# Kernel optimization log

Measured on AMD Instinct MI355X. Metric: run time of the kernel, lower is better.

## Reference

```python
import jax, jax.numpy as jnp
import numpy as np

B, S, D, E, K = 4, 2048, 2048, 64, 2

def setup_inputs() -> dict:
    key = jax.random.key(0)
    k1, k2, k3, k4 = jax.random.split(key, 4)
    x = jax.random.normal(k1, (B, S, D), dtype=jnp.float32)
    W = jax.random.normal(k2, (E, D), dtype=jnp.float32) * 0.02  # gate_linear.weight
    noise_weight = jax.random.normal(k3, (E,), dtype=jnp.float32) * 0.02
    noise = jax.random.normal(k4, (B, S, E), dtype=jnp.float32)  # torch.randn_like(logits), noisy_std=1.0
    return {"x": x, "W": W, "noise_weight": noise_weight, "noise": noise, "k": K}

def reference(x, W, noise_weight, noise, k):
    # logits = x @ W.T  -> [B, S, E]
    logits = jnp.einsum('bsd,ed->bse', x, W)
    # noise injection: randn * noisy_std(=1.0) * noise_weight (per-expert scale)
    logits_noisy = logits + noise * noise_weight
    # top-k over experts
    top_vals, top_idx = jax.lax.top_k(logits_noisy, k)  # [B, S, k]
    # softmax over a tensor that is -inf everywhere except the top-k slots is
    # exactly: zeros everywhere, softmax(top_vals) scattered into the top-k slots.
    probs = jax.nn.softmax(top_vals, axis=-1)  # [B, S, k]
    n_tok = B * S
    rows = jnp.arange(n_tok)[:, None]  # [n_tok, 1]
    gated = jnp.zeros((n_tok, E), dtype=logits.dtype)
    gated = gated.at[rows, top_idx.reshape(n_tok, k)].set(probs.reshape(n_tok, k))
    gated = gated.reshape(B, S, E)
    return gated, top_idx, top_vals
```

## Files before the change

kernel.cpp:

```cpp
#include <hip/hip_runtime.h>
#include <math.h>

#define NTOK 8192
#define DDIM 2048
#define NEXP 64
#define MT   16
#define ASTR 72
#define CSTR 68

#define GATED_SZ (NTOK * NEXP)
#define IDX_OFF  GATED_SZ
#define VALS_OFF (GATED_SZ + NTOK * 2)

#define NKSTEP (DDIM / 32)
#define NTILE  (NEXP / 16)
#define BFRAG_HALVES ((size_t)NKSTEP * NTILE * 64 * 8)

typedef _Float16 f16x8 __attribute__((ext_vector_type(8)));
typedef _Float16 f16x4 __attribute__((ext_vector_type(4)));
typedef float    f32x4 __attribute__((ext_vector_type(4)));

__global__ void pack_b_kernel(const float* __restrict__ W,
                              _Float16* __restrict__ Bh,
                              _Float16* __restrict__ Bl)
{
    const int tid  = blockIdx.x * blockDim.x + threadIdx.x;
    const int lane = tid & 63;
    const int fid  = tid >> 6;
    const int ks   = fid >> 2;
    const int nt   = fid & 3;
    const int e    = nt * 16 + (lane & 15);
    const int k    = ks * 32 + (lane >> 4) * 8;
    const float* src = W + (size_t)e * DDIM + k;

    f16x8 hi, lo;
#pragma unroll
    for (int j = 0; j < 8; ++j) {
        const float v = src[j];
        const _Float16 h = (_Float16)v;
        hi[j] = h;
        lo[j] = (_Float16)((v - (float)h) * 4096.f);
    }
    *(f16x8*)(Bh + (size_t)tid * 8) = hi;
    *(f16x8*)(Bl + (size_t)tid * 8) = lo;
}

#define BFRAG(base, ks, nt) \
    (*(const f16x8*)((base) + ((((size_t)(ks)) * 4 + (nt)) * 64 + lane) * 8))

static __device__ __forceinline__ void cvt_hilo4(float4 v, f16x4& h4, f16x4& l4)
{
    const float vv[4] = {v.x, v.y, v.z, v.w};
#pragma unroll
    for (int j = 0; j < 4; ++j) {
        const _Float16 hh = (_Float16)vv[j];
        h4[j] = hh;
        l4[j] = (_Float16)((vv[j] - (float)hh) * 4096.f);
    }
}

__global__ __launch_bounds__(512, 4) void gate_kernel(
    const float* __restrict__ x,
    const _Float16* __restrict__ Bh,
    const _Float16* __restrict__ Bl,
    const float* __restrict__ noise_w,
    const float* __restrict__ noise,
    float* __restrict__ out)
{
    __shared__ __align__(16) char smem_raw[8 * 2 * MT * ASTR * 2];

    const int tid  = threadIdx.x;
    const int lane = tid & 63;
    const int w    = __builtin_amdgcn_readfirstlane(tid >> 6);
    const int tokBase = blockIdx.x * MT;

    const int q = lane >> 4;
    const int m = lane & 15;

    _Float16* xs = (_Float16*)smem_raw + (size_t)w * (2 * MT * ASTR);

    const float* xw = x + (size_t)tokBase * DDIM + (size_t)w * 256;

    const float nwv = noise_w[lane];
    const float nz0 = noise[(size_t)(tokBase + w * 2)     * NEXP + lane];
    const float nz1 = noise[(size_t)(tokBase + w * 2 + 1) * NEXP + lane];

    f32x4 acc_hh[4], acc_lo[4];
#pragma unroll
    for (int nt = 0; nt < 4; ++nt) {
        acc_hh[nt] = (f32x4){0.f, 0.f, 0.f, 0.f};
        acc_lo[nt] = (f32x4){0.f, 0.f, 0.f, 0.f};
    }

#define LOADSUB(buf, s)                                                      \
    _Pragma("unroll")                                                        \
    for (int p = 0; p < 4; ++p) {                                            \
        buf[p] = *(const float4*)(xw + (size_t)(p * 4 + q) * DDIM            \
                                  + (s) * 64 + m * 4);                       \
    }

#define STAGESUB(buf)                                                        \
    _Pragma("unroll")                                                        \
    for (int p = 0; p < 4; ++p) {                                            \
        f16x4 h4, l4;                                                        \
        cvt_hilo4(buf[p], h4, l4);                                           \
        const int off = (p * 4 + q) * ASTR + m * 4;                          \
        *(f16x4*)&xs[off] = h4;                                              \
        *(f16x4*)&xs[MT * ASTR + off] = l4;                                  \
    }

#define COMPUTESUB(s)                                                        \
    _Pragma("unroll")                                                        \
    for (int stp = 0; stp < 2; ++stp) {                                      \
        const int ks = w * 8 + (s) * 2 + stp;                                \
        const f16x8 ah = *(const f16x8*)&xs[m * ASTR + stp * 32 + q * 8];    \
        const f16x8 al = *(const f16x8*)&xs[MT * ASTR + m * ASTR + stp * 32 + q * 8]; \
        _Pragma("unroll")                                                    \
        for (int nt = 0; nt < 4; ++nt) {                                     \
            const f16x8 bh = BFRAG(Bh, ks, nt);                              \
            const f16x8 bl = BFRAG(Bl, ks, nt);                              \
            acc_hh[nt] = __builtin_amdgcn_mfma_f32_16x16x32_f16(ah, bh, acc_hh[nt], 0, 0, 0); \
            acc_lo[nt] = __builtin_amdgcn_mfma_f32_16x16x32_f16(ah, bl, acc_lo[nt], 0, 0, 0); \
            acc_lo[nt] = __builtin_amdgcn_mfma_f32_16x16x32_f16(al, bh, acc_lo[nt], 0, 0, 0); \
        }                                                                    \
    }

    float4 rA[4], rB[4];
    LOADSUB(rA, 0)
    LOADSUB(rB, 1)
    STAGESUB(rA)
    LOADSUB(rA, 2)
    COMPUTESUB(0)
    STAGESUB(rB)
    LOADSUB(rB, 3)
    COMPUTESUB(1)
    STAGESUB(rA)
    COMPUTESUB(2)
    STAGESUB(rB)
    COMPUTESUB(3)

#undef LOADSUB
#undef STAGESUB
#undef COMPUTESUB

    __syncthreads();
    float* cbuf = (float*)smem_raw;

#pragma unroll
    for (int nt = 0; nt < 4; ++nt) {
        const int e = nt * 16 + m;
#pragma unroll
        for (int r = 0; r < 4; ++r) {
            const int t = q * 4 + r;
            cbuf[((w * MT) + t) * CSTR + e] = acc_hh[nt][r] + acc_lo[nt][r] * (1.f / 4096.f);
        }
    }
    __syncthreads();

#pragma unroll
    for (int i = 0; i < 2; ++i) {
        const int t   = w * 2 + i;
        const int tok = tokBase + t;
        const int e   = lane;

        float v = 0.f;
#pragma unroll
        for (int p = 0; p < 8; ++p)
            v += cbuf[((p * MT) + t) * CSTR + e];
        v += (i ? nz1 : nz0) * nwv;

        float m1 = v; int i1 = e;
#pragma unroll
        for (int sh = 32; sh > 0; sh >>= 1) {
            float ov = __shfl_xor(m1, sh, 64);
            int   oi = __shfl_xor(i1, sh, 64);
            if (ov > m1 || (ov == m1 && oi < i1)) { m1 = ov; i1 = oi; }
        }
        float vm = (e == i1) ? -INFINITY : v;
        float m2 = vm; int i2 = e;
#pragma unroll
        for (int sh = 32; sh > 0; sh >>= 1) {
            float ov = __shfl_xor(m2, sh, 64);
            int   oi = __shfl_xor(i2, sh, 64);
            if (ov > m2 || (ov == m2 && oi < i2)) { m2 = ov; i2 = oi; }
        }

        const float e2  = expf(m2 - m1);
        const float inv = 1.f / (1.f + e2);
        const float p1  = inv;
        const float p2  = e2 * inv;

        float gval = 0.f;
        if (e == i1) gval = p1;
        else if (e == i2) gval = p2;
        out[(size_t)tok * NEXP + e] = gval;

        if (lane == 0) {
            out[IDX_OFF  + tok * 2 + 0] = (float)i1;
            out[IDX_OFF  + tok * 2 + 1] = (float)i2;
            out[VALS_OFF + tok * 2 + 0] = m1;
            out[VALS_OFF + tok * 2 + 1] = m2;
        }
    }
}

extern "C" void kernel_launch(void* const* d_in, const int* in_sizes, int n_in,
                              void* d_out, int out_size, void* d_ws, size_t ws_size,
                              hipStream_t stream) {
    const float* x     = (const float*)d_in[0];
    const float* W     = (const float*)d_in[1];
    const float* nw    = (const float*)d_in[2];
    const float* noise = (const float*)d_in[3];
    float* out = (float*)d_out;

    _Float16* Bh = (_Float16*)d_ws;
    _Float16* Bl = Bh + BFRAG_HALVES;

    hipLaunchKernelGGL(pack_b_kernel, dim3(64), dim3(256), 0, stream, W, Bh, Bl);

    hipLaunchKernelGGL(gate_kernel, dim3(NTOK / MT), dim3(512), 0, stream,
                       x, Bh, Bl, nw, noise, out);
}
```

Baseline: 112.8 us.

## Double token tile to 32 and split K across 16 waves per block

Each block now handles 32 tokens with 1024 threads (16 waves), and each wave covers a 128-wide K slice with two 16-row M tiles. The point is to reuse each loaded W fragment across twice as many tokens, which halves the global/L2 traffic for B per token. In exchange the K-split reduction now sums 16 partials, shared memory grows, and load/compute pipelining drops from double to single buffering. Launching 1024-thread blocks with launch_bounds(1024,4) may also limit registers and occupancy.

```diff
diff --git a/kernel.cpp b/kernel.cpp
--- a/kernel.cpp
+++ b/kernel.cpp
@@ -4,9 +4,11 @@
 #define NTOK 8192
 #define DDIM 2048
 #define NEXP 64
-#define MT   16
-#define ASTR 72
-#define CSTR 68
+#define MT   32
+#define ASTR 40
+#define XLO  (32 * ASTR)
+#define WST  (2 * 32 * ASTR)
+#define CSTR 66
 
 #define GATED_SZ (NTOK * NEXP)
 #define IDX_OFF  GATED_SZ
@@ -59,7 +61,7 @@
     }
 }
 
-__global__ __launch_bounds__(512, 4) void gate_kernel(
+__global__ __launch_bounds__(1024, 4) void gate_kernel(
     const float* __restrict__ x,
     const _Float16* __restrict__ Bh,
     const _Float16* __restrict__ Bl,
@@ -67,7 +69,7 @@
     const float* __restrict__ noise,
     float* __restrict__ out)
 {
-    __shared__ __align__(16) char smem_raw[8 * 2 * MT * ASTR * 2];
+    __shared__ __align__(16) char smem_raw[16 * 32 * CSTR * 4];
 
     const int tid  = threadIdx.x;
     const int lane = tid & 63;
@@ -77,66 +79,72 @@
     const int q = lane >> 4;
     const int m = lane & 15;
 
-    _Float16* xs = (_Float16*)smem_raw + (size_t)w * (2 * MT * ASTR);
-
-    const float* xw = x + (size_t)tokBase * DDIM + (size_t)w * 256;
+    _Float16* xs = (_Float16*)smem_raw + (size_t)w * WST;
+
+    const int srow = tid & 0 ? 0 : (lane >> 3);
+    const int scol = (lane & 7) * 4;
+    const float* xw = x + (size_t)tokBase * DDIM + (size_t)w * 128;
 
     const float nwv = noise_w[lane];
     const float nz0 = noise[(size_t)(tokBase + w * 2)     * NEXP + lane];
     const float nz1 = noise[(size_t)(tokBase + w * 2 + 1) * NEXP + lane];
 
-    f32x4 acc_hh[4], acc_lo[4];
-#pragma unroll
-    for (int nt = 0; nt < 4; ++nt) {
-        acc_hh[nt] = (f32x4){0.f, 0.f, 0.f, 0.f};
-        acc_lo[nt] = (f32x4){0.f, 0.f, 0.f, 0.f};
-    }
-
-#define LOADSUB(buf, s)                                                      \
+    f32x4 acc_hh[2][4], acc_lo[2][4];
+#pragma unroll
+    for (int mt = 0; mt < 2; ++mt)
+#pragma unroll
+        for (int nt = 0; nt < 4; ++nt) {
+            acc_hh[mt][nt] = (f32x4){0.f, 0.f, 0.f, 0.f};
+            acc_lo[mt][nt] = (f32x4){0.f, 0.f, 0.f, 0.f};
+        }
+
+#define LOADSUB(s)                                                           \
     _Pragma("unroll")                                                        \
     for (int p = 0; p < 4; ++p) {                                            \
-        buf[p] = *(const float4*)(xw + (size_t)(p * 4 + q) * DDIM            \
-                                  + (s) * 64 + m * 4);                       \
-    }
-
-#define STAGESUB(buf)                                                        \
+        rA[p] = *(const float4*)(xw + (size_t)(p * 8 + srow) * DDIM          \
+                                 + (s) * 32 + scol);                         \
+    }
+
+#define STAGESUB()                                                           \
     _Pragma("unroll")                                                        \
     for (int p = 0; p < 4; ++p) {                                            \
         f16x4 h4, l4;                                                        \
-        cvt_hilo4(buf[p], h4, l4);                                           \
-        const int off = (p * 4 + q) * ASTR + m * 4;                          \
+        cvt_hilo4(rA[p], h4, l4);                                            \
+        const int off = (p * 8 + srow) * ASTR + scol;                        \
         *(f16x4*)&xs[off] = h4;                                              \
-        *(f16x4*)&xs[MT * ASTR + off] = l4;                                  \
+        *(f16x4*)&xs[XLO + off] = l4;                                        \
     }
 
 #define COMPUTESUB(s)                                                        \
-    _Pragma("unroll")                                                        \
-    for (int stp = 0; stp < 2; ++stp) {                                      \
-        const int ks = w * 8 + (s) * 2 + stp;                                \
-        const f16x8 ah = *(const f16x8*)&xs[m * ASTR + stp * 32 + q * 8];    \
-        const f16x8 al = *(const f16x8*)&xs[MT * ASTR + m * ASTR + stp * 32 + q * 8]; \
+    {                                                                        \
+        const int ks = w * 4 + (s);                                          \
         _Pragma("unroll")                                                    \
-        for (int nt = 0; nt < 4; ++nt) {                                     \
-            const f16x8 bh = BFRAG(Bh, ks, nt);                              \
-            const f16x8 bl = BFRAG(Bl, ks, nt);                              \
-            acc_hh[nt] = __builtin_amdgcn_mfma_f32_16x16x32_f16(ah, bh, acc_hh[nt], 0, 0, 0); \
-            acc_lo[nt] = __builtin_amdgcn_mfma_f32_16x16x32_f16(ah, bl, acc_lo[nt], 0, 0, 0); \
-            acc_lo[nt] = __builtin_amdgcn_mfma_f32_16x16x32_f16(al, bh, acc_lo[nt], 0, 0, 0); \
+        for (int mt = 0; mt < 2; ++mt) {                                     \
+            const f16x8 ah = *(const f16x8*)&xs[(mt * 16 + m) * ASTR + q * 8]; \
+            const f16x8 al = *(const f16x8*)&xs[XLO + (mt * 16 + m) * ASTR + q * 8]; \
+            _Pragma("unroll")                                                \
+            for (int nt = 0; nt < 4; ++nt) {                                 \
+                const f16x8 bh = BFRAG(Bh, ks, nt);                          \
+                const f16x8 bl = BFRAG(Bl, ks, nt);                          \
+                acc_hh[mt][nt] = __builtin_amdgcn_mfma_f32_16x16x32_f16(ah, bh, acc_hh[mt][nt], 0, 0, 0); \
+                acc_lo[mt][nt] = __builtin_amdgcn_mfma_f32_16x16x32_f16(ah, bl, acc_lo[mt][nt], 0, 0, 0); \
+                acc_lo[mt][nt] = __builtin_amdgcn_mfma_f32_16x16x32_f16(al, bh, acc_lo[mt][nt], 0, 0, 0); \
+            }                                                                \
         }                                                                    \
     }
 
-    float4 rA[4], rB[4];
-    LOADSUB(rA, 0)
-    LOADSUB(rB, 1)
-    STAGESUB(rA)
-    LOADSUB(rA, 2)
+    float4 rA[4];
+    LOADSUB(0)
+    STAGESUB()
+    LOADSUB(1)
     COMPUTESUB(0)
-    STAGESUB(rB)
-    LOADSUB(rB, 3)
+    STAGESUB()
+    LOADSUB(2)
     COMPUTESUB(1)
-    STAGESUB(rA)
+    STAGESUB()
+    LOADSUB(3)
     COMPUTESUB(2)
-    STAGESUB(rB)
+    STAGESUB()
     COMPUTESUB(3)
 
 #undef LOADSUB
@@ -147,14 +155,17 @@
     float* cbuf = (float*)smem_raw;
 
 #pragma unroll
-    for (int nt = 0; nt < 4; ++nt) {
-        const int e = nt * 16 + m;
-#pragma unroll
-        for (int r = 0; r < 4; ++r) {
-            const int t = q * 4 + r;
-            cbuf[((w * MT) + t) * CSTR + e] = acc_hh[nt][r] + acc_lo[nt][r] * (1.f / 4096.f);
-        }
-    }
+    for (int mt = 0; mt < 2; ++mt)
+#pragma unroll
+        for (int nt = 0; nt < 4; ++nt) {
+            const int e = nt * 16 + m;
+#pragma unroll
+            for (int r = 0; r < 4; ++r) {
+                const int t = mt * 16 + q * 4 + r;
+                cbuf[((w * MT) + t) * CSTR + e] =
+                    acc_hh[mt][nt][r] + acc_lo[mt][nt][r] * (1.f / 4096.f);
+            }
+        }
     __syncthreads();
 
 #pragma unroll
@@ -165,7 +176,7 @@
 
         float v = 0.f;
 #pragma unroll
-        for (int p = 0; p < 8; ++p)
+        for (int p = 0; p < 16; ++p)
             v += cbuf[((p * MT) + t) * CSTR + e];
         v += (i ? nz1 : nz0) * nwv;
 
@@ -218,6 +229,6 @@
 
     hipLaunchKernelGGL(pack_b_kernel, dim3(64), dim3(256), 0, stream, W, Bh, Bl);
 
-    hipLaunchKernelGGL(gate_kernel, dim3(NTOK / MT), dim3(512), 0, stream,
+    hipLaunchKernelGGL(gate_kernel, dim3(NTOK / MT), dim3(1024), 0, stream,
                        x, Bh, Bl, nw, noise, out);
 }
```

New measurement: 115.7 us. 1.03x slower.

## Split reduction dimension across 16 waves per block instead of 8

Applied to the files above, without the earlier changes.

Doubles the block to 1024 threads so each wave covers a 128-element K slice instead of 256, with one token per wave in the top-k epilogue. This raises the number of waves in flight per token tile to hide global load latency. In exchange, each wave keeps only one load buffer and loses the prior double-buffered load/stage/compute overlap. Shared memory doubles, the cross-wave reduction adds 16 partials instead of 8, and the launch bounds request 8 blocks of 1024 threads, which may squeeze registers.

```diff
diff --git a/kernel.cpp b/kernel.cpp
--- a/kernel.cpp
+++ b/kernel.cpp
@@ -5,6 +5,7 @@
 #define DDIM 2048
 #define NEXP 64
 #define MT   16
+#define NW   16
 #define ASTR 72
 #define CSTR 68
 
@@ -59,7 +60,7 @@
     }
 }
 
-__global__ __launch_bounds__(512, 4) void gate_kernel(
+__global__ __launch_bounds__(1024, 8) void gate_kernel(
     const float* __restrict__ x,
     const _Float16* __restrict__ Bh,
     const _Float16* __restrict__ Bl,
@@ -67,7 +68,7 @@
     const float* __restrict__ noise,
     float* __restrict__ out)
 {
-    __shared__ __align__(16) char smem_raw[8 * 2 * MT * ASTR * 2];
+    __shared__ __align__(16) char smem_raw[NW * 2 * MT * ASTR * 2];
 
     const int tid  = threadIdx.x;
     const int lane = tid & 63;
@@ -79,11 +80,10 @@
 
     _Float16* xs = (_Float16*)smem_raw + (size_t)w * (2 * MT * ASTR);
 
-    const float* xw = x + (size_t)tokBase * DDIM + (size_t)w * 256;
+    const float* xw = x + (size_t)tokBase * DDIM + (size_t)w * 128;
 
     const float nwv = noise_w[lane];
-    const float nz0 = noise[(size_t)(tokBase + w * 2)     * NEXP + lane];
-    const float nz1 = noise[(size_t)(tokBase + w * 2 + 1) * NEXP + lane];
+    const float nz  = noise[(size_t)(tokBase + w) * NEXP + lane];
 
     f32x4 acc_hh[4], acc_lo[4];
 #pragma unroll
@@ -92,18 +92,18 @@
         acc_lo[nt] = (f32x4){0.f, 0.f, 0.f, 0.f};
     }
 
-#define LOADSUB(buf, s)                                                      \
+#define LOADSUB(s)                                                           \
     _Pragma("unroll")                                                        \
     for (int p = 0; p < 4; ++p) {                                            \
-        buf[p] = *(const float4*)(xw + (size_t)(p * 4 + q) * DDIM            \
+        rA[p] = *(const float4*)(xw + (size_t)(p * 4 + q) * DDIM             \
                                   + (s) * 64 + m * 4);                       \
     }
 
-#define STAGESUB(buf)                                                        \
+#define STAGESUB()                                                           \
     _Pragma("unroll")                                                        \
     for (int p = 0; p < 4; ++p) {                                            \
         f16x4 h4, l4;                                                        \
-        cvt_hilo4(buf[p], h4, l4);                                           \
+        cvt_hilo4(rA[p], h4, l4);                                            \
         const int off = (p * 4 + q) * ASTR + m * 4;                          \
         *(f16x4*)&xs[off] = h4;                                              \
         *(f16x4*)&xs[MT * ASTR + off] = l4;                                  \
@@ -112,7 +112,7 @@
 #define COMPUTESUB(s)                                                        \
     _Pragma("unroll")                                                        \
     for (int stp = 0; stp < 2; ++stp) {                                      \
-        const int ks = w * 8 + (s) * 2 + stp;                                \
+        const int ks = w * 4 + (s) * 2 + stp;                                \
         const f16x8 ah = *(const f16x8*)&xs[m * ASTR + stp * 32 + q * 8];    \
         const f16x8 al = *(const f16x8*)&xs[MT * ASTR + m * ASTR + stp * 32 + q * 8]; \
         _Pragma("unroll")                                                    \
@@ -125,19 +125,13 @@
         }                                                                    \
     }
 
-    float4 rA[4], rB[4];
-    LOADSUB(rA, 0)
-    LOADSUB(rB, 1)
-    STAGESUB(rA)
-    LOADSUB(rA, 2)
+    float4 rA[4];
+    LOADSUB(0)
+    STAGESUB()
+    LOADSUB(1)
     COMPUTESUB(0)
-    STAGESUB(rB)
-    LOADSUB(rB, 3)
+    STAGESUB()
     COMPUTESUB(1)
-    STAGESUB(rA)
-    COMPUTESUB(2)
-    STAGESUB(rB)
-    COMPUTESUB(3)
 
 #undef LOADSUB
 #undef STAGESUB
@@ -152,22 +146,22 @@
 #pragma unroll
         for (int r = 0; r < 4; ++r) {
             const int t = q * 4 + r;
-            cbuf[((w * MT) + t) * CSTR + e] = acc_hh[nt][r] + acc_lo[nt][r] * (1.f / 4096.f);
+            cbuf[((w * MT) + t) * CSTR + e] =
+                acc_hh[nt][r] + acc_lo[nt][r] * (1.f / 4096.f);
         }
     }
     __syncthreads();
 
-#pragma unroll
-    for (int i = 0; i < 2; ++i) {
-        const int t   = w * 2 + i;
+    {
+        const int t   = w;
         const int tok = tokBase + t;
         const int e   = lane;
 
         float v = 0.f;
 #pragma unroll
-        for (int p = 0; p < 8; ++p)
+        for (int p = 0; p < 16; ++p)
             v += cbuf[((p * MT) + t) * CSTR + e];
-        v += (i ? nz1 : nz0) * nwv;
+        v += nz * nwv;
 
         float m1 = v; int i1 = e;
 #pragma unroll
@@ -218,6 +212,6 @@
 
     hipLaunchKernelGGL(pack_b_kernel, dim3(64), dim3(256), 0, stream, W, Bh, Bl);
 
-    hipLaunchKernelGGL(gate_kernel, dim3(NTOK / MT), dim3(512), 0, stream,
+    hipLaunchKernelGGL(gate_kernel, dim3(NTOK / MT), dim3(1024), 0, stream,
                        x, Bh, Bl, nw, noise, out);
 }
```

Measured after the change: 135.6 us. +20.2%, slower.

## Fuse W hi/lo fp16 split into gate kernel, drop pack kernel

Applied to the files above, without the earlier changes.

Removes the separate pack_b_kernel launch and its workspace round-trip. Each wave now reads fp32 W directly from global memory and converts it to hi/lo fp16 MFMA fragments inside the compute loop. This saves a kernel launch and a dependency between kernels. The cost is redundant W loads and conversions in every block (512 blocks), twice the bytes per fragment, and less coalesced per-lane loads from W.

```diff
diff --git a/kernel.cpp b/kernel.cpp
--- a/kernel.cpp
+++ b/kernel.cpp
@@ -12,41 +12,9 @@
 #define IDX_OFF  GATED_SZ
 #define VALS_OFF (GATED_SZ + NTOK * 2)
 
-#define NKSTEP (DDIM / 32)
-#define NTILE  (NEXP / 16)
-#define BFRAG_HALVES ((size_t)NKSTEP * NTILE * 64 * 8)
-
 typedef _Float16 f16x8 __attribute__((ext_vector_type(8)));
 typedef _Float16 f16x4 __attribute__((ext_vector_type(4)));
 typedef float    f32x4 __attribute__((ext_vector_type(4)));
-
-__global__ void pack_b_kernel(const float* __restrict__ W,
-                              _Float16* __restrict__ Bh,
-                              _Float16* __restrict__ Bl)
-{
-    const int tid  = blockIdx.x * blockDim.x + threadIdx.x;
-    const int lane = tid & 63;
-    const int fid  = tid >> 6;
-    const int ks   = fid >> 2;
-    const int nt   = fid & 3;
-    const int e    = nt * 16 + (lane & 15);
-    const int k    = ks * 32 + (lane >> 4) * 8;
-    const float* src = W + (size_t)e * DDIM + k;
-
-    f16x8 hi, lo;
-#pragma unroll
-    for (int j = 0; j < 8; ++j) {
-        const float v = src[j];
-        const _Float16 h = (_Float16)v;
-        hi[j] = h;
-        lo[j] = (_Float16)((v - (float)h) * 4096.f);
-    }
-    *(f16x8*)(Bh + (size_t)tid * 8) = hi;
-    *(f16x8*)(Bl + (size_t)tid * 8) = lo;
-}
-
-#define BFRAG(base, ks, nt) \
-    (*(const f16x8*)((base) + ((((size_t)(ks)) * 4 + (nt)) * 64 + lane) * 8))
 
 static __device__ __forceinline__ void cvt_hilo4(float4 v, f16x4& h4, f16x4& l4)
 {
@@ -59,10 +27,21 @@
     }
 }
 
+static __device__ __forceinline__ void cvt_hilo8(float4 v0, float4 v1,
+                                                 f16x8& h8, f16x8& l8)
+{
+    const float vv[8] = {v0.x, v0.y, v0.z, v0.w, v1.x, v1.y, v1.z, v1.w};
+#pragma unroll
+    for (int j = 0; j < 8; ++j) {
+        const _Float16 hh = (_Float16)vv[j];
+        h8[j] = hh;
+        l8[j] = (_Float16)((vv[j] - (float)hh) * 4096.f);
+    }
+}
+
 __global__ __launch_bounds__(512, 4) void gate_kernel(
     const float* __restrict__ x,
-    const _Float16* __restrict__ Bh,
-    const _Float16* __restrict__ Bl,
+    const float* __restrict__ W,
     const float* __restrict__ noise_w,
     const float* __restrict__ noise,
     float* __restrict__ out)
@@ -80,6 +59,7 @@
     _Float16* xs = (_Float16*)smem_raw + (size_t)w * (2 * MT * ASTR);
 
     const float* xw = x + (size_t)tokBase * DDIM + (size_t)w * 256;
+    const float* wb = W + (size_t)m * DDIM + (size_t)w * 256 + q * 8;
 
     const float nwv = noise_w[lane];
     const float nz0 = noise[(size_t)(tokBase + w * 2)     * NEXP + lane];
@@ -112,13 +92,16 @@
 #define COMPUTESUB(s)                                                        \
     _Pragma("unroll")                                                        \
     for (int stp = 0; stp < 2; ++stp) {                                      \
-        const int ks = w * 8 + (s) * 2 + stp;                                \
+        const int ko = ((s) * 2 + stp) * 32;                                 \
         const f16x8 ah = *(const f16x8*)&xs[m * ASTR + stp * 32 + q * 8];    \
         const f16x8 al = *(const f16x8*)&xs[MT * ASTR + m * ASTR + stp * 32 + q * 8]; \
         _Pragma("unroll")                                                    \
         for (int nt = 0; nt < 4; ++nt) {                                     \
-            const f16x8 bh = BFRAG(Bh, ks, nt);                              \
-            const f16x8 bl = BFRAG(Bl, ks, nt);                              \
+            const float* wsrc = wb + (size_t)(nt * 16) * DDIM + ko;          \
+            const float4 w0 = *(const float4*)(wsrc);                        \
+            const float4 w1 = *(const float4*)(wsrc + 4);                    \
+            f16x8 bh, bl;                                                    \
+            cvt_hilo8(w0, w1, bh, bl);                                       \
             acc_hh[nt] = __builtin_amdgcn_mfma_f32_16x16x32_f16(ah, bh, acc_hh[nt], 0, 0, 0); \
             acc_lo[nt] = __builtin_amdgcn_mfma_f32_16x16x32_f16(ah, bl, acc_lo[nt], 0, 0, 0); \
             acc_lo[nt] = __builtin_amdgcn_mfma_f32_16x16x32_f16(al, bh, acc_lo[nt], 0, 0, 0); \
@@ -152,7 +135,8 @@
 #pragma unroll
         for (int r = 0; r < 4; ++r) {
             const int t = q * 4 + r;
-            cbuf[((w * MT) + t) * CSTR + e] = acc_hh[nt][r] + acc_lo[nt][r] * (1.f / 4096.f);
+            cbuf[((w * MT) + t) * CSTR + e] =
+                acc_hh[nt][r] + acc_lo[nt][r] * (1.f / 4096.f);
         }
     }
     __syncthreads();
@@ -212,12 +196,8 @@
     const float* nw    = (const float*)d_in[2];
     const float* noise = (const float*)d_in[3];
     float* out = (float*)d_out;
-
-    _Float16* Bh = (_Float16*)d_ws;
-    _Float16* Bl = Bh + BFRAG_HALVES;
-
-    hipLaunchKernelGGL(pack_b_kernel, dim3(64), dim3(256), 0, stream, W, Bh, Bl);
+    (void)d_ws; (void)ws_size;
 
     hipLaunchKernelGGL(gate_kernel, dim3(NTOK / MT), dim3(512), 0, stream,
-                       x, Bh, Bl, nw, noise, out);
-}
+                       x, W, nw, noise, out);
+}
```

After: 128.5 us. +13.9%, slower.
